# Optimization experiments

Measured on AMD Instinct MI355X. Metric: run time of the kernel, lower is better.

Reference implementation:

```python
import jax, jax.numpy as jnp
import numpy as np

B, LL, LP, D, H, TOPK = 4, 256, 256, 256, 128, 100


def setup_inputs() -> dict:
    key = jax.random.key(0)
    ks = jax.random.split(key, 16)
    s = 0.02
    return {
        "l_tok": jax.random.normal(ks[0], (B, LL, D), jnp.float32),
        "p_tok": jax.random.normal(ks[1], (B, LP, D), jnp.float32),
        "l_pad": jax.random.bernoulli(ks[2], 0.1, (B, LL)),
        "p_pad": jax.random.bernoulli(ks[3], 0.1, (B, LP)),
        "Wl": jax.random.normal(ks[4], (D, D), jnp.float32) * s,
        "bl": jnp.zeros((D,), jnp.float32),
        "Wp": jax.random.normal(ks[5], (D, D), jnp.float32) * s,
        "bp": jnp.zeros((D,), jnp.float32),
        "W1": jax.random.normal(ks[6], (H, 4 * D), jnp.float32) * s,
        "b1": jnp.zeros((H,), jnp.float32),
        "W2": jax.random.normal(ks[7], (H, H), jnp.float32) * s,
        "b2": jnp.zeros((H,), jnp.float32),
        "W3": jax.random.normal(ks[8], (1, H), jnp.float32) * s,
        "b3": jnp.zeros((1,), jnp.float32),
    }


def reference(l_tok, p_tok, l_pad, p_pad, Wl, bl, Wp, bp, W1, b1, W2, b2, W3, b3):
    # Linear projections (torch Linear: x @ W.T + b)
    l = jnp.einsum("bld,ed->ble", l_tok, Wl) + bl  # [B,Ll,D]
    p = jnp.einsum("bpd,ed->bpe", p_tok, Wp) + bp  # [B,Lp,D]

    le = jnp.broadcast_to(l[:, :, None, :], (B, LL, LP, D))
    pe = jnp.broadcast_to(p[:, None, :, :], (B, LL, LP, D))
    pair_feat = jnp.concatenate([le, pe, le * pe, jnp.abs(le - pe)], axis=-1)  # [B,Ll,Lp,4D]

    gelu = lambda x: jax.nn.gelu(x, approximate=False)  # torch nn.GELU default (erf)
    h = gelu(jnp.einsum("blpf,hf->blph", pair_feat, W1) + b1)
    h = gelu(jnp.einsum("blph,gh->blpg", h, W2) + b2)
    pair_logit = (jnp.einsum("blph,oh->blpo", h, W3) + b3)[..., 0]  # [B,Ll,Lp]

    pair_logit = jnp.nan_to_num(pair_logit, nan=0.0, posinf=20.0, neginf=-20.0)

    valid = (~l_pad)[:, :, None] & (~p_pad)[:, None, :]  # [B,Ll,Lp]
    pair_logit = jnp.where(valid, pair_logit, -20.0)
    pair_prob = jax.nn.sigmoid(pair_logit)

    flat = pair_logit.reshape(B, -1)
    k_top = min(TOPK, LL * LP)
    topv, _ = jax.lax.top_k(flat, k_top)  # [B,k]
    w = jax.nn.softmax(topv, axis=-1)
    logit = jnp.sum(w * topv, axis=-1)  # [B]
    return logit, pair_logit, pair_prob
```

## Files before the change

### kernel.cpp

```cpp
#include <hip/hip_runtime.h>

#define BB 4
#define LLL 256
#define LPP 256
#define DDIM 256
#define HH 128

typedef _Float16 f16;
typedef f16 f16x8 __attribute__((ext_vector_type(8)));
typedef f16 f16x4 __attribute__((ext_vector_type(4)));
typedef float floatx4 __attribute__((ext_vector_type(4)));

__device__ __forceinline__ float gelu_f(float x) {
    return x * __builtin_amdgcn_rcpf(1.f + __expf(-1.702f * x));
}
__device__ __forceinline__ float sigmoid_f(float x) {
    return __builtin_amdgcn_rcpf(1.f + __expf(-x));
}
__device__ __forceinline__ f16x8 habs8(f16x8 v) {
    uint4 u = __builtin_bit_cast(uint4, v);
    u.x &= 0x7fff7fffu; u.y &= 0x7fff7fffu; u.z &= 0x7fff7fffu; u.w &= 0x7fff7fffu;
    return __builtin_bit_cast(f16x8, u);
}
__device__ __forceinline__ unsigned okey(float f) {
    unsigned u = __float_as_uint(f);
    return (u & 0x80000000u) ? ~u : (u | 0x80000000u);
}

#define TK_H0(b) (tk + (b) * 256)
#define TK_H1(b) (tk + 1024 + (b) * 256)
#define TK_S1(b) ((float*)(tk + 2048) + (b))
#define TK_S2(b) ((float*)(tk + 2052) + (b))
#define TK_CA(b) (tk + 2056 + (b))
#define TK_CB(b) (tk + 2060 + (b))
#define TK_CC(b) (tk + 2064 + (b))
#define TK_INTS 2068

__global__ __launch_bounds__(256) void prep_proj(
    const float* __restrict__ l_tok, const float* __restrict__ p_tok,
    const float* __restrict__ Wl, const float* __restrict__ Wp,
    const float* __restrict__ bl, const float* __restrict__ bp,
    f16* __restrict__ proj) {
    __shared__ __align__(16) char sm[2 * 64 * 80];
    f16* As = (f16*)sm;
    f16* Bs = (f16*)(sm + 64 * 80);
    int tid = threadIdx.x;
    int m0 = blockIdx.x * 64, n0 = blockIdx.y * 64;
    bool isP = (m0 >= 1024);
    const float* Asrc = isP ? (p_tok + (size_t)(m0 - 1024) * DDIM) : (l_tok + (size_t)m0 * DDIM);
    const float* Wsrc = isP ? Wp : Wl;
    const float* bias = isP ? bp : bl;
    int row = tid >> 2, seg = tid & 3;
    int w = tid >> 6, lane = tid & 63;
    int m16 = lane & 15, quad = lane >> 4;
    int wm = w & 1, wn = w >> 1;
    floatx4 acc[2][2];
#pragma unroll
    for (int a = 0; a < 2; ++a)
#pragma unroll
        for (int c = 0; c < 2; ++c) acc[a][c] = (floatx4)0.f;
    for (int k0 = 0; k0 < DDIM; k0 += 32) {
        float4 f0 = *(const float4*)(Asrc + row * DDIM + k0 + seg * 8);
        float4 f1 = *(const float4*)(Asrc + row * DDIM + k0 + seg * 8 + 4);
        f16x8 av;
        av[0] = (f16)f0.x; av[1] = (f16)f0.y; av[2] = (f16)f0.z; av[3] = (f16)f0.w;
        av[4] = (f16)f1.x; av[5] = (f16)f1.y; av[6] = (f16)f1.z; av[7] = (f16)f1.w;
        *(f16x8*)(As + row * 40 + seg * 8) = av;
        float4 g0 = *(const float4*)(Wsrc + (n0 + row) * DDIM + k0 + seg * 8);
        float4 g1 = *(const float4*)(Wsrc + (n0 + row) * DDIM + k0 + seg * 8 + 4);
        f16x8 bv;
        bv[0] = (f16)g0.x; bv[1] = (f16)g0.y; bv[2] = (f16)g0.z; bv[3] = (f16)g0.w;
        bv[4] = (f16)g1.x; bv[5] = (f16)g1.y; bv[6] = (f16)g1.z; bv[7] = (f16)g1.w;
        *(f16x8*)(Bs + row * 40 + seg * 8) = bv;
        __syncthreads();
        f16x8 afr[2], bfr[2];
#pragma unroll
        for (int t = 0; t < 2; ++t)
            afr[t] = *(const f16x8*)(As + (wm * 32 + t * 16 + m16) * 40 + quad * 8);
#pragma unroll
        for (int t = 0; t < 2; ++t)
            bfr[t] = *(const f16x8*)(Bs + (wn * 32 + t * 16 + m16) * 40 + quad * 8);
#pragma unroll
        for (int a = 0; a < 2; ++a)
#pragma unroll
            for (int c = 0; c < 2; ++c)
                acc[a][c] = __builtin_amdgcn_mfma_f32_16x16x32_f16(afr[a], bfr[c], acc[a][c], 0, 0, 0);
        __syncthreads();
    }
#pragma unroll
    for (int c = 0; c < 2; ++c) {
        int col = n0 + wn * 32 + c * 16 + m16;
        float bv = bias[col];
#pragma unroll
        for (int a = 0; a < 2; ++a) {
            int rbase = m0 + wm * 32 + a * 16 + quad * 4;
#pragma unroll
            for (int i = 0; i < 4; ++i)
                proj[(size_t)(rbase + i) * DDIM + col] = (f16)(acc[a][c][i] + bv);
        }
    }
}

__global__ __launch_bounds__(256) void prep_ab(
    const f16* __restrict__ proj, const float* __restrict__ W1,
    const float* __restrict__ W2, float* __restrict__ ABt,
    f16* __restrict__ w1g, f16* __restrict__ w2g, int* __restrict__ tk) {
    int tid = threadIdx.x;
    if (blockIdx.x >= 32) {
        int idx = ((blockIdx.x - 32) * 2 + blockIdx.y) * 256 + tid;
        if (idx < 8192) {
            int m16 = idx & 15, quad = (idx >> 4) & 3, th = (idx >> 6) & 7;
            int cd = (idx >> 9) & 1, ds = idx >> 10;
            int h = th * 16 + m16;
            const float* src = W1 + (size_t)h * 1024 + 512 + cd * 256 + ds * 32 + quad * 8;
            f16x8 v;
#pragma unroll
            for (int j = 0; j < 8; ++j) v[j] = (f16)src[j];
            *(f16x8*)(w1g + (size_t)idx * 8) = v;
        } else if (idx < 8192 + 2048) {
            int c = idx - 8192;
            int m16 = c & 15, quad = (c >> 4) & 3, tg = (c >> 6) & 7, ks = c >> 9;
            int g = tg * 16 + m16;
            f16x8 v;
#pragma unroll
            for (int j = 0; j < 8; ++j) v[j] = (f16)W2[g * HH + j * 16 + ks * 4 + quad];
            *(f16x8*)(w2g + (size_t)c * 8) = v;
        } else {
            int zid = idx - 10240;
            if (zid >= 0 && zid < TK_INTS) tk[zid] = 0;
        }
        return;
    }
    __shared__ __align__(16) char sm[2 * 64 * 80];
    f16* As = (f16*)sm;
    f16* Bs = (f16*)(sm + 64 * 80);
    int m0 = blockIdx.x * 64, n0 = blockIdx.y * 64;
    bool isP = (m0 >= 1024);
    int koff = isP ? 256 : 0;
    int row = tid >> 2, seg = tid & 3;
    int w = tid >> 6, lane = tid & 63;
    int m16 = lane & 15, quad = lane >> 4;
    int wm = w & 1, wn = w >> 1;
    floatx4 acc[2][2];
#pragma unroll
    for (int a = 0; a < 2; ++a)
#pragma unroll
        for (int c = 0; c < 2; ++c) acc[a][c] = (floatx4)0.f;
    for (int k0 = 0; k0 < DDIM; k0 += 32) {
        f16x8 av = *(const f16x8*)(proj + (size_t)(m0 + row) * DDIM + k0 + seg * 8);
        *(f16x8*)(As + row * 40 + seg * 8) = av;
        float4 g0 = *(const float4*)(W1 + (size_t)(n0 + row) * 1024 + koff + k0 + seg * 8);
        float4 g1 = *(const float4*)(W1 + (size_t)(n0 + row) * 1024 + koff + k0 + seg * 8 + 4);
        f16x8 bv;
        bv[0] = (f16)g0.x; bv[1] = (f16)g0.y; bv[2] = (f16)g0.z; bv[3] = (f16)g0.w;
        bv[4] = (f16)g1.x; bv[5] = (f16)g1.y; bv[6] = (f16)g1.z; bv[7] = (f16)g1.w;
        *(f16x8*)(Bs + row * 40 + seg * 8) = bv;
        __syncthreads();
        f16x8 afr[2], bfr[2];
#pragma unroll
        for (int t = 0; t < 2; ++t)
            afr[t] = *(const f16x8*)(As + (wm * 32 + t * 16 + m16) * 40 + quad * 8);
#pragma unroll
        for (int t = 0; t < 2; ++t)
            bfr[t] = *(const f16x8*)(Bs + (wn * 32 + t * 16 + m16) * 40 + quad * 8);
#pragma unroll
        for (int a = 0; a < 2; ++a)
#pragma unroll
            for (int c = 0; c < 2; ++c)
                acc[a][c] = __builtin_amdgcn_mfma_f32_16x16x32_f16(afr[a], bfr[c], acc[a][c], 0, 0, 0);
        __syncthreads();
    }
#pragma unroll
    for (int c = 0; c < 2; ++c) {
        int col = n0 + wn * 32 + c * 16 + m16;
#pragma unroll
        for (int a = 0; a < 2; ++a) {
            int rbase = m0 + wm * 32 + a * 16 + quad * 4;
#pragma unroll
            for (int i = 0; i < 4; ++i)
                ABt[(size_t)col * 2048 + rbase + i] = acc[a][c][i];
        }
    }
}

#define H1_STRIDE 272
#define SM_PLOG 139264
#define SM_TOTAL 141312

__global__ __launch_bounds__(512, 2) void pair_main(
    const f16* __restrict__ proj, const float* __restrict__ ABt,
    const f16* __restrict__ w1g, const f16* __restrict__ w2g,
    const float* __restrict__ b1, const float* __restrict__ b2,
    const float* __restrict__ W3, const float* __restrict__ b3,
    const int* __restrict__ l_pad, const int* __restrict__ p_pad,
    float* __restrict__ out) {
    __shared__ __align__(16) char sm[SM_TOTAL];
    int tid = threadIdx.x;
    int lane = tid & 63, w = tid >> 6;
    int m16 = lane & 15, quad = lane >> 4;
    int wp = w & 3, wh = w >> 2;
    int p0 = wp * 64, h0 = wh * 64;
    int b = blockIdx.y;
    int l0 = blockIdx.x * 2;
    int ml0 = b * LLL + l0;
    float* outPL = out + 4;
    float* outPR = out + 4 + BB * LLL * LPP;

    bool pad0 = (l_pad[ml0] != 0), pad1 = (l_pad[ml0 + 1] != 0);
    if (pad0 && pad1) {
        float pr = sigmoid_f(-20.f);
        if (tid < 512) {
            int j = tid >> 8, p = tid & 255;
            outPL[(size_t)(ml0 + j) * LPP + p] = -20.f;
            outPR[(size_t)(ml0 + j) * LPP + p] = pr;
        }
        return;
    }

    float* plog = (float*)(sm + SM_PLOG);

#pragma unroll
    for (int r = 0; r < 16; ++r) {
        int c = tid + r * 512;
        *(f16x8*)(sm + c * 16) = *(const f16x8*)(w1g + (size_t)c * 8);
    }
    if (tid < 512) plog[tid] = 0.f;

    floatx4 acc[2][4][4];
    {
        float av[2][4];
#pragma unroll
        for (int th = 0; th < 4; ++th) {
            int hh = h0 + th * 16 + m16;
            float base = b1[hh];
            av[0][th] = ABt[(size_t)hh * 2048 + ml0] + base;
            av[1][th] = ABt[(size_t)hh * 2048 + ml0 + 1] + base;
        }
#pragma unroll
        for (int tp = 0; tp < 4; ++tp) {
            int rp = p0 + tp * 16 + quad * 4;
#pragma unroll
            for (int th = 0; th < 4; ++th) {
                int hh = h0 + th * 16 + m16;
                floatx4 bp4 = *(const floatx4*)(ABt + (size_t)hh * 2048 + 1024 + b * LPP + rp);
#pragma unroll
                for (int j = 0; j < 2; ++j) {
                    floatx4 a;
#pragma unroll
                    for (int i = 0; i < 4; ++i) a[i] = bp4[i] + av[j][th];
                    acc[j][tp][th] = a;
                }
            }
        }
    }
    __syncthreads();

    {
        const f16* Lr0 = proj + (size_t)ml0 * DDIM + quad * 8;
        const f16* Lr1 = Lr0 + DDIM;
        const f16* Prl[4];
#pragma unroll
        for (int tp = 0; tp < 4; ++tp)
            Prl[tp] = proj + (size_t)(1024 + b * LPP + p0 + tp * 16 + m16) * DDIM + quad * 8;

        f16x8 lv0 = *(const f16x8*)(Lr0);
        f16x8 lv1 = *(const f16x8*)(Lr1);
        f16x8 pv[4];
#pragma unroll
        for (int tp = 0; tp < 4; ++tp) pv[tp] = *(const f16x8*)(Prl[tp]);

        for (int ds = 0; ds < 8; ++ds) {
            f16x8 nlv0, nlv1, npv[4];
            if (ds < 7) {
                nlv0 = *(const f16x8*)(Lr0 + (ds + 1) * 32);
                nlv1 = *(const f16x8*)(Lr1 + (ds + 1) * 32);
#pragma unroll
                for (int tp = 0; tp < 4; ++tp)
                    npv[tp] = *(const f16x8*)(Prl[tp] + (ds + 1) * 32);
            }
            const char* wb = sm + (size_t)(ds * 2) * 8192 + (wh * 4) * 1024 + quad * 256 + m16 * 16;
            {
                f16x8 x[2][4];
#pragma unroll
                for (int tp = 0; tp < 4; ++tp) {
                    x[0][tp] = lv0 * pv[tp];
                    x[1][tp] = lv1 * pv[tp];
                }
#pragma unroll
                for (int th = 0; th < 4; ++th) {
                    f16x8 bf = *(const f16x8*)(wb + th * 1024);
#pragma unroll
                    for (int j = 0; j < 2; ++j)
#pragma unroll
                        for (int tp = 0; tp < 4; ++tp)
                            acc[j][tp][th] = __builtin_amdgcn_mfma_f32_16x16x32_f16(x[j][tp], bf, acc[j][tp][th], 0, 0, 0);
                }
            }
            {
                f16x8 x[2][4];
#pragma unroll
                for (int tp = 0; tp < 4; ++tp) {
                    x[0][tp] = habs8(lv0 - pv[tp]);
                    x[1][tp] = habs8(lv1 - pv[tp]);
                }
#pragma unroll
                for (int th = 0; th < 4; ++th) {
                    f16x8 bf = *(const f16x8*)(wb + 8192 + th * 1024);
#pragma unroll
                    for (int j = 0; j < 2; ++j)
#pragma unroll
                        for (int tp = 0; tp < 4; ++tp)
                            acc[j][tp][th] = __builtin_amdgcn_mfma_f32_16x16x32_f16(x[j][tp], bf, acc[j][tp][th], 0, 0, 0);
                }
            }
            lv0 = nlv0; lv1 = nlv1;
#pragma unroll
            for (int tp = 0; tp < 4; ++tp) pv[tp] = npv[tp];
        }
    }
    __syncthreads();

#pragma unroll
    for (int j = 0; j < 2; ++j) {
        char* h1s = sm + j * (256 * H1_STRIDE);
#pragma unroll
        for (int tp = 0; tp < 4; ++tp) {
#pragma unroll
            for (int i = 0; i < 4; ++i) {
                f16x4 hv;
#pragma unroll
                for (int th = 0; th < 4; ++th) hv[th] = (f16)gelu_f(acc[j][tp][th][i]);
                int p = p0 + tp * 16 + quad * 4 + i;
                *(f16x4*)(h1s + p * H1_STRIDE + m16 * 16 + wh * 8) = hv;
            }
        }
    }
    __syncthreads();

    float b2v[4], w3v[4];
#pragma unroll
    for (int th = 0; th < 4; ++th) {
        int g = h0 + th * 16 + m16;
        b2v[th] = b2[g];
        w3v[th] = W3[g];
    }
    floatx4 acc2[2][4][4];
#pragma unroll
    for (int j = 0; j < 2; ++j)
#pragma unroll
        for (int tp = 0; tp < 4; ++tp)
#pragma unroll
            for (int th = 0; th < 4; ++th) {
                floatx4 a;
                a[0] = a[1] = a[2] = a[3] = b2v[th];
                acc2[j][tp][th] = a;
            }
#pragma unroll
    for (int ks = 0; ks < 4; ++ks) {
        f16x8 af[2][4];
#pragma unroll
        for (int j = 0; j < 2; ++j)
#pragma unroll
            for (int tp = 0; tp < 4; ++tp)
                af[j][tp] = *(const f16x8*)(sm + j * (256 * H1_STRIDE) +
                                            (p0 + tp * 16 + m16) * H1_STRIDE + ks * 64 + quad * 16);
#pragma unroll
        for (int th = 0; th < 4; ++th) {
            f16x8 bf = *(const f16x8*)(w2g + (size_t)(((ks * 8 + wh * 4 + th) * 4 + quad) * 16 + m16) * 8);
#pragma unroll
            for (int j = 0; j < 2; ++j)
#pragma unroll
                for (int tp = 0; tp < 4; ++tp)
                    acc2[j][tp][th] = __builtin_amdgcn_mfma_f32_16x16x32_f16(af[j][tp], bf, acc2[j][tp][th], 0, 0, 0);
        }
    }

#pragma unroll
    for (int j = 0; j < 2; ++j) {
        float part[16];
#pragma unroll
        for (int q = 0; q < 16; ++q) part[q] = 0.f;
#pragma unroll
        for (int tp = 0; tp < 4; ++tp)
#pragma unroll
            for (int th = 0; th < 4; ++th)
#pragma unroll
                for (int i = 0; i < 4; ++i)
                    part[tp * 4 + i] += w3v[th] * gelu_f(acc2[j][tp][th][i]);
#pragma unroll
        for (int mask = 1; mask <= 8; mask <<= 1)
#pragma unroll
            for (int q = 0; q < 16; ++q) part[q] += __shfl_xor(part[q], mask, 64);
        if (m16 == 0) {
#pragma unroll
            for (int tp = 0; tp < 4; ++tp)
#pragma unroll
                for (int i = 0; i < 4; ++i)
                    atomicAdd(&plog[j * 256 + p0 + tp * 16 + quad * 4 + i], part[tp * 4 + i]);
        }
    }
    __syncthreads();

    if (tid < 512) {
        int j = tid >> 8, p = tid & 255;
        int ml = ml0 + j;
        float pl;
        if (l_pad[ml] != 0) {
            pl = -20.f;
        } else {
            pl = plog[tid] + b3[0];
            if (__builtin_isnan(pl)) pl = 0.f;
            else if (__builtin_isinf(pl)) pl = pl > 0.f ? 20.f : -20.f;
            if (p_pad[b * LPP + p] != 0) pl = -20.f;
        }
        outPL[(size_t)ml * LPP + p] = pl;
        outPR[(size_t)ml * LPP + p] = sigmoid_f(pl);
    }
}

__global__ __launch_bounds__(256) void tk_all(const float* __restrict__ pl,
                                              int* __restrict__ tk,
                                              float* __restrict__ out) {
    __shared__ int s[258];
    __shared__ int h[256];
    __shared__ float red[8];
    int tid = threadIdx.x, b = blockIdx.y;
    int lane = tid & 63, wv = tid >> 6;
    float4 t = ((const float4*)(pl + (size_t)b * 65536 + blockIdx.x * 1024))[tid];

    h[tid] = 0;
    __syncthreads();
#pragma unroll
    for (int c = 0; c < 4; ++c) atomicAdd(&h[okey((&t.x)[c]) >> 24], 1);
    __syncthreads();
    if (h[tid]) atomicAdd(&TK_H0(b)[tid], h[tid]);
    __threadfence();
    if (tid == 0) {
        atomicAdd(TK_CA(b), 1);
        while (atomicAdd(TK_CA(b), 0) < (int)gridDim.x) __builtin_amdgcn_s_sleep(2);
    }
    __syncthreads();

    s[tid] = atomicAdd(&TK_H0(b)[tid], 0);
    h[tid] = 0;
    __syncthreads();
    for (int off = 1; off < 256; off <<= 1) {
        int v = (tid + off < 256) ? s[tid + off] : 0;
        __syncthreads();
        s[tid] += v;
        __syncthreads();
    }
    {
        int nxt = (tid < 255) ? s[tid + 1] : 0;
        if (s[tid] >= 100 && nxt < 100) { s[256] = tid; s[257] = 100 - nxt; }
    }
    __syncthreads();
    unsigned pref0 = (unsigned)s[256];
    int rem0 = s[257];
    float s1 = 0.f, s2 = 0.f;
#pragma unroll
    for (int c = 0; c < 4; ++c) {
        float v = (&t.x)[c];
        unsigned key = okey(v);
        unsigned hi = key >> 24;
        if (hi > pref0) {
            float e = __expf(v);
            s1 += e;
            s2 += e * v;
        } else if (hi == pref0) {
            atomicAdd(&h[(key >> 16) & 255], 1);
        }
    }
    __syncthreads();
    if (h[tid]) atomicAdd(&TK_H1(b)[tid], h[tid]);
    for (int off = 32; off > 0; off >>= 1) {
        s1 += __shfl_xor(s1, off, 64);
        s2 += __shfl_xor(s2, off, 64);
    }
    if (lane == 0) { red[wv] = s1; red[4 + wv] = s2; }
    __syncthreads();
    if (tid == 0) {
        float a = red[0] + red[1] + red[2] + red[3];
        float bs = red[4] + red[5] + red[6] + red[7];
        if (a != 0.f) {
            atomicAdd(TK_S1(b), a);
            atomicAdd(TK_S2(b), bs);
        }
        __threadfence();
        atomicAdd(TK_CB(b), 1);
        while (atomicAdd(TK_CB(b), 0) < (int)gridDim.x) __builtin_amdgcn_s_sleep(2);
    }
    __syncthreads();

    s[tid] = atomicAdd(&TK_H1(b)[tid], 0);
    __syncthreads();
    for (int off = 1; off < 256; off <<= 1) {
        int v = (tid + off < 256) ? s[tid + off] : 0;
        __syncthreads();
        s[tid] += v;
        __syncthreads();
    }
    {
        int nxt = (tid < 255) ? s[tid + 1] : 0;
        if (s[tid] >= rem0 && nxt < rem0) { s[256] = tid; s[257] = rem0 - nxt; }
    }
    __syncthreads();
    unsigned pref1 = (unsigned)s[256];
    int rem1 = s[257];
    s1 = 0.f; s2 = 0.f;
#pragma unroll
    for (int c = 0; c < 4; ++c) {
        float v = (&t.x)[c];
        unsigned key = okey(v);
        if ((key >> 24) == pref0 && ((key >> 16) & 255) > pref1) {
            float e = __expf(v);
            s1 += e;
            s2 += e * v;
        }
    }
    for (int off = 32; off > 0; off >>= 1) {
        s1 += __shfl_xor(s1, off, 64);
        s2 += __shfl_xor(s2, off, 64);
    }
    if (lane == 0) { red[wv] = s1; red[4 + wv] = s2; }
    __syncthreads();
    if (tid == 0) {
        float a = red[0] + red[1] + red[2] + red[3];
        float bs = red[4] + red[5] + red[6] + red[7];
        if (a != 0.f) {
            atomicAdd(TK_S1(b), a);
            atomicAdd(TK_S2(b), bs);
        }
        __threadfence();
        int done = atomicAdd(TK_CC(b), 1);
        if (done == (int)gridDim.x - 1) {
            float S1 = atomicAdd(TK_S1(b), 0.f);
            float S2 = atomicAdd(TK_S2(b), 0.f);
            unsigned key = (pref0 << 24) | (pref1 << 16) | 0x8000u;
            unsigned bits = (key & 0x80000000u) ? (key & 0x7fffffffu) : ~key;
            float vT = __uint_as_float(bits);
            float e = __expf(vT);
            S1 += (float)rem1 * e;
            S2 += (float)rem1 * e * vT;
            out[b] = S2 * __builtin_amdgcn_rcpf(S1);
        }
    }
}

extern "C" void kernel_launch(void* const* d_in, const int* in_sizes, int n_in,
                              void* d_out, int out_size, void* d_ws, size_t ws_size,
                              hipStream_t stream) {
    const float* l_tok = (const float*)d_in[0];
    const float* p_tok = (const float*)d_in[1];
    const int* l_pad = (const int*)d_in[2];
    const int* p_pad = (const int*)d_in[3];
    const float* Wl = (const float*)d_in[4];
    const float* bl = (const float*)d_in[5];
    const float* Wp = (const float*)d_in[6];
    const float* bp = (const float*)d_in[7];
    const float* W1 = (const float*)d_in[8];
    const float* b1 = (const float*)d_in[9];
    const float* W2 = (const float*)d_in[10];
    const float* b2 = (const float*)d_in[11];
    const float* W3 = (const float*)d_in[12];
    const float* b3 = (const float*)d_in[13];
    float* out = (float*)d_out;

    char* ws = (char*)d_ws;
    f16* proj = (f16*)ws;
    float* ABt = (float*)(ws + (size_t)2048 * 256 * 2);
    f16* w1g = (f16*)(ws + (size_t)2048 * 256 * 2 + (size_t)128 * 2048 * 4);
    f16* w2g = (f16*)((char*)w1g + (size_t)8192 * 16);
    int* tk = (int*)((char*)w2g + (size_t)2048 * 16);

    prep_proj<<<dim3(32, 4), 256, 0, stream>>>(l_tok, p_tok, Wl, Wp, bl, bp, proj);
    prep_ab<<<dim3(57, 2), 256, 0, stream>>>(proj, W1, W2, ABt, w1g, w2g, tk);
    pair_main<<<dim3(LLL / 2, BB), 512, 0, stream>>>(proj, ABt, w1g, w2g, b1, b2, W3, b3,
                                                     l_pad, p_pad, out);
    tk_all<<<dim3(64, BB), 256, 0, stream>>>(out + 4, tk, out);
}
```

Before: 207.3 us.

## Use packed fp16 polynomial GELU and single-block-per-batch top-k selection

The sigmoid-based GELU in both MLP layers is replaced by a packed half-precision polynomial approximation clamped between min(x,0) and max(x,0), which removes the exp and reciprocal per element. The top-k reduction moves from a 64-block-per-batch kernel that synchronised through global atomics and spin-waits to one 1024-thread block per batch, using warp-replicated shared histograms with run-length batching of atomics. This also drops the workspace zeroing from prep_ab. The fp16 polynomial is less accurate than the previous approximation. One block per batch uses only four CUs for the top-k pass.

```diff
diff --git a/kernel.cpp b/kernel.cpp
--- a/kernel.cpp
+++ b/kernel.cpp
@@ -9,13 +9,29 @@
 typedef _Float16 f16;
 typedef f16 f16x8 __attribute__((ext_vector_type(8)));
 typedef f16 f16x4 __attribute__((ext_vector_type(4)));
+typedef f16 f16x2 __attribute__((ext_vector_type(2)));
 typedef float floatx4 __attribute__((ext_vector_type(4)));
 
+__device__ __forceinline__ float sigmoid_f(float x) {
+    return __builtin_amdgcn_rcpf(1.f + __expf(-x));
+}
 __device__ __forceinline__ float gelu_f(float x) {
     return x * __builtin_amdgcn_rcpf(1.f + __expf(-1.702f * x));
 }
-__device__ __forceinline__ float sigmoid_f(float x) {
-    return __builtin_amdgcn_rcpf(1.f + __expf(-x));
+__device__ __forceinline__ f16x2 gelu_pk2(float a, float b) {
+    f16x2 x;
+    x[0] = (f16)a; x[1] = (f16)b;
+    f16x2 x2 = x * x;
+    f16x2 E = x2 * (f16)0.00562f + (f16)-0.06235f;
+    E = E * x2 + (f16)0.39803f;
+    E = E * x2;
+    f16x2 g = x * (f16)0.5f + E;
+    f16x2 z = {(f16)0.f, (f16)0.f};
+    f16x2 lo = __builtin_elementwise_min(x, z);
+    f16x2 hi = __builtin_elementwise_max(x, z);
+    g = __builtin_elementwise_max(g, lo);
+    g = __builtin_elementwise_min(g, hi);
+    return g;
 }
 __device__ __forceinline__ f16x8 habs8(f16x8 v) {
     uint4 u = __builtin_bit_cast(uint4, v);
@@ -26,15 +42,6 @@
     unsigned u = __float_as_uint(f);
     return (u & 0x80000000u) ? ~u : (u | 0x80000000u);
 }
-
-#define TK_H0(b) (tk + (b) * 256)
-#define TK_H1(b) (tk + 1024 + (b) * 256)
-#define TK_S1(b) ((float*)(tk + 2048) + (b))
-#define TK_S2(b) ((float*)(tk + 2052) + (b))
-#define TK_CA(b) (tk + 2056 + (b))
-#define TK_CB(b) (tk + 2060 + (b))
-#define TK_CC(b) (tk + 2064 + (b))
-#define TK_INTS 2068
 
 __global__ __launch_bounds__(256) void prep_proj(
     const float* __restrict__ l_tok, const float* __restrict__ p_tok,
@@ -104,7 +111,7 @@
 __global__ __launch_bounds__(256) void prep_ab(
     const f16* __restrict__ proj, const float* __restrict__ W1,
     const float* __restrict__ W2, float* __restrict__ ABt,
-    f16* __restrict__ w1g, f16* __restrict__ w2g, int* __restrict__ tk) {
+    f16* __restrict__ w1g, f16* __restrict__ w2g) {
     int tid = threadIdx.x;
     if (blockIdx.x >= 32) {
         int idx = ((blockIdx.x - 32) * 2 + blockIdx.y) * 256 + tid;
@@ -125,9 +132,6 @@
 #pragma unroll
             for (int j = 0; j < 8; ++j) v[j] = (f16)W2[g * HH + j * 16 + ks * 4 + quad];
             *(f16x8*)(w2g + (size_t)c * 8) = v;
-        } else {
-            int zid = idx - 10240;
-            if (zid >= 0 && zid < TK_INTS) tk[zid] = 0;
         }
         return;
     }
@@ -327,9 +331,10 @@
         for (int tp = 0; tp < 4; ++tp) {
 #pragma unroll
             for (int i = 0; i < 4; ++i) {
+                f16x2 g01 = gelu_pk2(acc[j][tp][0][i], acc[j][tp][1][i]);
+                f16x2 g23 = gelu_pk2(acc[j][tp][2][i], acc[j][tp][3][i]);
                 f16x4 hv;
-#pragma unroll
-                for (int th = 0; th < 4; ++th) hv[th] = (f16)gelu_f(acc[j][tp][th][i]);
+                hv[0] = g01[0]; hv[1] = g01[1]; hv[2] = g23[0]; hv[3] = g23[1];
                 int p = p0 + tp * 16 + quad * 4 + i;
                 *(f16x4*)(h1s + p * H1_STRIDE + m16 * 16 + wh * 8) = hv;
             }
@@ -383,10 +388,14 @@
 #pragma unroll
         for (int tp = 0; tp < 4; ++tp)
 #pragma unroll
-            for (int th = 0; th < 4; ++th)
-#pragma unroll
-                for (int i = 0; i < 4; ++i)
-                    part[tp * 4 + i] += w3v[th] * gelu_f(acc2[j][tp][th][i]);
+            for (int th = 0; th < 4; ++th) {
+                f16x2 gA = gelu_pk2(acc2[j][tp][th][0], acc2[j][tp][th][1]);
+                f16x2 gB = gelu_pk2(acc2[j][tp][th][2], acc2[j][tp][th][3]);
+                part[tp * 4 + 0] += w3v[th] * (float)gA[0];
+                part[tp * 4 + 1] += w3v[th] * (float)gA[1];
+                part[tp * 4 + 2] += w3v[th] * (float)gB[0];
+                part[tp * 4 + 3] += w3v[th] * (float)gB[1];
+            }
 #pragma unroll
         for (int mask = 1; mask <= 8; mask <<= 1)
 #pragma unroll
@@ -418,132 +427,133 @@
     }
 }
 
-__global__ __launch_bounds__(256) void tk_all(const float* __restrict__ pl,
-                                              int* __restrict__ tk,
-                                              float* __restrict__ out) {
+__global__ __launch_bounds__(1024) void tk_one(const float* __restrict__ pl,
+                                               float* __restrict__ out) {
+    __shared__ int hist[16 * 256];
     __shared__ int s[258];
-    __shared__ int h[256];
-    __shared__ float red[8];
-    int tid = threadIdx.x, b = blockIdx.y;
-    int lane = tid & 63, wv = tid >> 6;
-    float4 t = ((const float4*)(pl + (size_t)b * 65536 + blockIdx.x * 1024))[tid];
-
-    h[tid] = 0;
-    __syncthreads();
-#pragma unroll
-    for (int c = 0; c < 4; ++c) atomicAdd(&h[okey((&t.x)[c]) >> 24], 1);
-    __syncthreads();
-    if (h[tid]) atomicAdd(&TK_H0(b)[tid], h[tid]);
-    __threadfence();
-    if (tid == 0) {
-        atomicAdd(TK_CA(b), 1);
-        while (atomicAdd(TK_CA(b), 0) < (int)gridDim.x) __builtin_amdgcn_s_sleep(2);
-    }
-    __syncthreads();
-
-    s[tid] = atomicAdd(&TK_H0(b)[tid], 0);
-    h[tid] = 0;
+    __shared__ float red[32];
+    int tid = threadIdx.x, b = blockIdx.x;
+    int wv = tid >> 6, lane = tid & 63;
+    const float4* src = (const float4*)(pl + (size_t)b * 65536);
+
+#pragma unroll
+    for (int r = 0; r < 4; ++r) hist[tid + r * 1024] = 0;
+    __syncthreads();
+    {
+        int rep = wv * 256;
+        unsigned cb0 = 0xffffffffu, cb1 = 0xffffffffu;
+        int cc0 = 0, cc1 = 0;
+        for (int j = 0; j < 16; ++j) {
+            float4 t = src[tid + j * 1024];
+#pragma unroll
+            for (int c = 0; c < 4; ++c) {
+                unsigned bin = okey((&t.x)[c]) >> 24;
+                if (bin & 1) {
+                    if (bin == cb1) cc1++;
+                    else { if (cc1) atomicAdd(&hist[rep + cb1], cc1); cb1 = bin; cc1 = 1; }
+                } else {
+                    if (bin == cb0) cc0++;
+                    else { if (cc0) atomicAdd(&hist[rep + cb0], cc0); cb0 = bin; cc0 = 1; }
+                }
+            }
+        }
+        if (cc0) atomicAdd(&hist[rep + cb0], cc0);
+        if (cc1) atomicAdd(&hist[rep + cb1], cc1);
+    }
+    __syncthreads();
+    if (tid < 256) {
+        int t0 = 0;
+#pragma unroll
+        for (int ww = 0; ww < 16; ++ww) t0 += hist[ww * 256 + tid];
+        s[tid] = t0;
+    }
     __syncthreads();
     for (int off = 1; off < 256; off <<= 1) {
-        int v = (tid + off < 256) ? s[tid + off] : 0;
-        __syncthreads();
-        s[tid] += v;
-        __syncthreads();
-    }
-    {
+        int v = 0;
+        if (tid < 256) v = (tid + off < 256) ? s[tid + off] : 0;
+        __syncthreads();
+        if (tid < 256) s[tid] += v;
+        __syncthreads();
+    }
+    if (tid < 256) {
         int nxt = (tid < 255) ? s[tid + 1] : 0;
         if (s[tid] >= 100 && nxt < 100) { s[256] = tid; s[257] = 100 - nxt; }
     }
     __syncthreads();
     unsigned pref0 = (unsigned)s[256];
     int rem0 = s[257];
+    __syncthreads();
+
+    hist[tid] = 0;
+    __syncthreads();
     float s1 = 0.f, s2 = 0.f;
-#pragma unroll
-    for (int c = 0; c < 4; ++c) {
-        float v = (&t.x)[c];
-        unsigned key = okey(v);
-        unsigned hi = key >> 24;
-        if (hi > pref0) {
-            float e = __expf(v);
-            s1 += e;
-            s2 += e * v;
-        } else if (hi == pref0) {
-            atomicAdd(&h[(key >> 16) & 255], 1);
-        }
-    }
-    __syncthreads();
-    if (h[tid]) atomicAdd(&TK_H1(b)[tid], h[tid]);
+    {
+        int rep = (wv & 3) * 256;
+        for (int j = 0; j < 16; ++j) {
+            float4 t = src[tid + j * 1024];
+#pragma unroll
+            for (int c = 0; c < 4; ++c) {
+                float v = (&t.x)[c];
+                unsigned key = okey(v);
+                unsigned hi = key >> 24;
+                if (hi > pref0) {
+                    float e = __expf(v);
+                    s1 += e;
+                    s2 += e * v;
+                } else if (hi == pref0) {
+                    atomicAdd(&hist[rep + ((key >> 16) & 255)], 1);
+                }
+            }
+        }
+    }
+    __syncthreads();
+    if (tid < 256)
+        s[tid] = hist[tid] + hist[256 + tid] + hist[512 + tid] + hist[768 + tid];
+    __syncthreads();
+    for (int off = 1; off < 256; off <<= 1) {
+        int v = 0;
+        if (tid < 256) v = (tid + off < 256) ? s[tid + off] : 0;
+        __syncthreads();
+        if (tid < 256) s[tid] += v;
+        __syncthreads();
+    }
+    if (tid < 256) {
+        int nxt = (tid < 255) ? s[tid + 1] : 0;
+        if (s[tid] >= rem0 && nxt < rem0) { s[256] = tid; s[257] = rem0 - nxt; }
+    }
+    __syncthreads();
+    unsigned pref1 = (unsigned)s[256];
+    int rem1 = s[257];
+
+    for (int j = 0; j < 16; ++j) {
+        float4 t = src[tid + j * 1024];
+#pragma unroll
+        for (int c = 0; c < 4; ++c) {
+            float v = (&t.x)[c];
+            unsigned key = okey(v);
+            if ((key >> 24) == pref0 && ((key >> 16) & 255) > pref1) {
+                float e = __expf(v);
+                s1 += e;
+                s2 += e * v;
+            }
+        }
+    }
     for (int off = 32; off > 0; off >>= 1) {
         s1 += __shfl_xor(s1, off, 64);
         s2 += __shfl_xor(s2, off, 64);
     }
-    if (lane == 0) { red[wv] = s1; red[4 + wv] = s2; }
+    if (lane == 0) { red[wv] = s1; red[16 + wv] = s2; }
     __syncthreads();
     if (tid == 0) {
-        float a = red[0] + red[1] + red[2] + red[3];
-        float bs = red[4] + red[5] + red[6] + red[7];
-        if (a != 0.f) {
-            atomicAdd(TK_S1(b), a);
-            atomicAdd(TK_S2(b), bs);
-        }
-        __threadfence();
-        atomicAdd(TK_CB(b), 1);
-        while (atomicAdd(TK_CB(b), 0) < (int)gridDim.x) __builtin_amdgcn_s_sleep(2);
-    }
-    __syncthreads();
-
-    s[tid] = atomicAdd(&TK_H1(b)[tid], 0);
-    __syncthreads();
-    for (int off = 1; off < 256; off <<= 1) {
-        int v = (tid + off < 256) ? s[tid + off] : 0;
-        __syncthreads();
-        s[tid] += v;
-        __syncthreads();
-    }
-    {
-        int nxt = (tid < 255) ? s[tid + 1] : 0;
-        if (s[tid] >= rem0 && nxt < rem0) { s[256] = tid; s[257] = rem0 - nxt; }
-    }
-    __syncthreads();
-    unsigned pref1 = (unsigned)s[256];
-    int rem1 = s[257];
-    s1 = 0.f; s2 = 0.f;
-#pragma unroll
-    for (int c = 0; c < 4; ++c) {
-        float v = (&t.x)[c];
-        unsigned key = okey(v);
-        if ((key >> 24) == pref0 && ((key >> 16) & 255) > pref1) {
-            float e = __expf(v);
-            s1 += e;
-            s2 += e * v;
-        }
-    }
-    for (int off = 32; off > 0; off >>= 1) {
-        s1 += __shfl_xor(s1, off, 64);
-        s2 += __shfl_xor(s2, off, 64);
-    }
-    if (lane == 0) { red[wv] = s1; red[4 + wv] = s2; }
-    __syncthreads();
-    if (tid == 0) {
-        float a = red[0] + red[1] + red[2] + red[3];
-        float bs = red[4] + red[5] + red[6] + red[7];
-        if (a != 0.f) {
-            atomicAdd(TK_S1(b), a);
-            atomicAdd(TK_S2(b), bs);
-        }
-        __threadfence();
-        int done = atomicAdd(TK_CC(b), 1);
-        if (done == (int)gridDim.x - 1) {
-            float S1 = atomicAdd(TK_S1(b), 0.f);
-            float S2 = atomicAdd(TK_S2(b), 0.f);
-            unsigned key = (pref0 << 24) | (pref1 << 16) | 0x8000u;
-            unsigned bits = (key & 0x80000000u) ? (key & 0x7fffffffu) : ~key;
-            float vT = __uint_as_float(bits);
-            float e = __expf(vT);
-            S1 += (float)rem1 * e;
-            S2 += (float)rem1 * e * vT;
-            out[b] = S2 * __builtin_amdgcn_rcpf(S1);
-        }
+        float S1 = 0.f, S2 = 0.f;
+        for (int i = 0; i < 16; ++i) { S1 += red[i]; S2 += red[16 + i]; }
+        unsigned key = (pref0 << 24) | (pref1 << 16) | 0x8000u;
+        unsigned bits = (key & 0x80000000u) ? (key & 0x7fffffffu) : ~key;
+        float vT = __uint_as_float(bits);
+        float e = __expf(vT);
+        S1 += (float)rem1 * e;
+        S2 += (float)rem1 * e * vT;
+        out[b] = S2 * __builtin_amdgcn_rcpf(S1);
     }
 }
 
@@ -571,11 +581,10 @@
     float* ABt = (float*)(ws + (size_t)2048 * 256 * 2);
     f16* w1g = (f16*)(ws + (size_t)2048 * 256 * 2 + (size_t)128 * 2048 * 4);
     f16* w2g = (f16*)((char*)w1g + (size_t)8192 * 16);
-    int* tk = (int*)((char*)w2g + (size_t)2048 * 16);
 
     prep_proj<<<dim3(32, 4), 256, 0, stream>>>(l_tok, p_tok, Wl, Wp, bl, bp, proj);
-    prep_ab<<<dim3(57, 2), 256, 0, stream>>>(proj, W1, W2, ABt, w1g, w2g, tk);
+    prep_ab<<<dim3(52, 2), 256, 0, stream>>>(proj, W1, W2, ABt, w1g, w2g);
     pair_main<<<dim3(LLL / 2, BB), 512, 0, stream>>>(proj, ABt, w1g, w2g, b1, b2, W3, b3,
                                                      l_pad, p_pad, out);
-    tk_all<<<dim3(64, BB), 256, 0, stream>>>(out + 4, tk, out);
-}
+    tk_one<<<BB, 1024, 0, stream>>>(out + 4, out);
+}
```

New measurement: 191.1 us. 7.8% less time.
